# Kernel tuning notes

Measured on AMD Instinct MI355X. Metric: run time of the kernel, lower is better.

## Reference

```python
import jax, jax.numpy as jnp
import numpy as np

EPS = 1e-6

def _rms_norm(x, w):
    # per-head RMSNorm over last dim (head_dim)
    var = jnp.mean(jnp.square(x), axis=-1, keepdims=True)
    return x * jax.lax.rsqrt(var + EPS) * w

def _linear(x, w, b):
    # torch nn.Linear: y = x @ W^T + b
    return jnp.einsum('bsd,od->bso', x, w) + b

def setup_inputs() -> dict:
    key = jax.random.key(0)
    ks = jax.random.split(key, 16)
    B, S, S_enc, D, H, HD = 1, 2048, 256, 1536, 24, 64
    w = lambda k: jax.random.normal(k, (D, D), dtype=jnp.float32) * 0.02
    return {
        'hidden_states': jax.random.normal(ks[0], (B, S, D), dtype=jnp.float32),
        'encoder_hidden_states': jax.random.normal(ks[1], (B, S_enc, D), dtype=jnp.float32),
        'attention_mask': jnp.zeros((B, 1, 1, S + S_enc), dtype=jnp.float32),
        'to_q_weight': w(ks[2]), 'to_q_bias': jnp.zeros((D,), jnp.float32),
        'to_k_weight': w(ks[3]), 'to_k_bias': jnp.zeros((D,), jnp.float32),
        'to_v_weight': w(ks[4]), 'to_v_bias': jnp.zeros((D,), jnp.float32),
        'norm_q_weight': jnp.ones((HD,), jnp.float32),
        'norm_k_weight': jnp.ones((HD,), jnp.float32),
        'add_q_proj_weight': w(ks[5]), 'add_q_proj_bias': jnp.zeros((D,), jnp.float32),
        'add_k_proj_weight': w(ks[6]), 'add_k_proj_bias': jnp.zeros((D,), jnp.float32),
        'add_v_proj_weight': w(ks[7]), 'add_v_proj_bias': jnp.zeros((D,), jnp.float32),
        'norm_added_q_weight': jnp.ones((HD,), jnp.float32),
        'norm_added_k_weight': jnp.ones((HD,), jnp.float32),
        'to_out_0_weight': w(ks[8]), 'to_out_0_bias': jnp.zeros((D,), jnp.float32),
        'to_add_out_weight': w(ks[9]), 'to_add_out_bias': jnp.zeros((D,), jnp.float32),
        'attn_heads': 24,
        'attn_head_dim': 64,
    }

def reference(hidden_states, encoder_hidden_states, attention_mask,
              to_q_weight, to_q_bias, to_k_weight, to_k_bias, to_v_weight, to_v_bias,
              norm_q_weight, norm_k_weight,
              add_q_proj_weight, add_q_proj_bias, add_k_proj_weight, add_k_proj_bias,
              add_v_proj_weight, add_v_proj_bias,
              norm_added_q_weight, norm_added_k_weight,
              to_out_0_weight, to_out_0_bias, to_add_out_weight, to_add_out_bias,
              attn_heads, attn_head_dim):
    B, S, D = hidden_states.shape
    S_enc = encoder_hidden_states.shape[1]
    H, HD = attn_heads, attn_head_dim
    scale = float(HD) ** -0.5

    def split_heads(x):  # [B,T,H*HD] -> [B,H,T,HD]
        return x.reshape(B, -1, H, HD).transpose(0, 2, 1, 3)

    # hidden-stream QKV + per-head RMSNorm on q,k
    q = _rms_norm(split_heads(_linear(hidden_states, to_q_weight, to_q_bias)), norm_q_weight)
    k = _rms_norm(split_heads(_linear(hidden_states, to_k_weight, to_k_bias)), norm_k_weight)
    v = split_heads(_linear(hidden_states, to_v_weight, to_v_bias))

    # encoder-stream QKV + per-head RMSNorm on q,k
    eq = _rms_norm(split_heads(_linear(encoder_hidden_states, add_q_proj_weight, add_q_proj_bias)), norm_added_q_weight)
    ek = _rms_norm(split_heads(_linear(encoder_hidden_states, add_k_proj_weight, add_k_proj_bias)), norm_added_k_weight)
    ev = split_heads(_linear(encoder_hidden_states, add_v_proj_weight, add_v_proj_bias))

    # concat streams along sequence: [B,H,S+S_enc,HD]
    q = jnp.concatenate([q, eq], axis=2)
    k = jnp.concatenate([k, ek], axis=2)
    v = jnp.concatenate([v, ev], axis=2)

    # SDPA with additive mask
    scores = jnp.einsum('bhqd,bhkd->bhqk', q, k) * scale + attention_mask
    probs = jax.nn.softmax(scores, axis=-1)
    out = jnp.einsum('bhqk,bhkd->bhqd', probs, v)  # [B,H,T,HD]
    out = out.transpose(0, 2, 1, 3).reshape(B, S + S_enc, H * HD)

    # split back into image / text streams, separate output projections
    attn_output = _linear(out[:, :S], to_out_0_weight, to_out_0_bias)
    context_attn_output = _linear(out[:, S:], to_add_out_weight, to_add_out_bias)
    del context_attn_output  # AttentionFunc returns only the hidden-stream output
    return attn_output
```

## Files before the change

### kernel.cpp

```cpp
#include <hip/hip_runtime.h>
#include <cstdint>


typedef __attribute__((ext_vector_type(8))) short s16x8;
typedef __attribute__((ext_vector_type(4))) float f32x4;

#define LOG2E 1.4426950408889634f

__device__ __forceinline__ short f2bf(float f) {
  union { float f; uint32_t u; } v; v.f = f;
  uint32_t r = v.u + 0x7FFFu + ((v.u >> 16) & 1u);
  return (short)(r >> 16);
}
__device__ __forceinline__ short f2bf_fast(float f) {
  union { float f; uint32_t u; } v; v.f = f;
  return (short)((v.u + 0x8000u) >> 16);
}

typedef uint32_t __attribute__((address_space(1)))* gas_u32;
typedef uint32_t __attribute__((address_space(3)))* las_u32;

__device__ __forceinline__ void gload_lds16(const short* g, short* l) {
  __builtin_amdgcn_global_load_lds((gas_u32)(g), (las_u32)(l), 16, 0, 0);
}

struct CvtSeg { const float* src; short* dst; int n4; };
struct CvtArgs { CvtSeg s[8]; };

__global__ __launch_bounds__(256) void cvt_bf16_kernel(CvtArgs a) {
  const int stride = gridDim.x * blockDim.x;
  const int tid = blockIdx.x * blockDim.x + threadIdx.x;
  for (int i = 0; i < 8; ++i) {
    const float4* src = (const float4*)a.s[i].src;
    short* dst = a.s[i].dst;
    const int n4 = a.s[i].n4;
    for (int j = tid; j < n4; j += stride) {
      float4 v = src[j];
      short4 o;
      o.x = f2bf(v.x); o.y = f2bf(v.y); o.z = f2bf(v.z); o.w = f2bf(v.w);
      *(short4*)(dst + (size_t)j * 4) = o;
    }
  }
}

enum { MODE_Q = 0, MODE_K = 1, MODE_V = 2, MODE_OUT = 3 };

struct GemmCfg {
  const short* A;
  const short* W;
  const float* bias;
  const float* normw;
  void* dst;
  int toff;
  int mode;
  int mtiles;
};
struct GemmArgs { GemmCfg c[5]; };

__global__ __launch_bounds__(256) void proj_gemm_kernel(GemmArgs args) {
  const GemmCfg cfg = args.c[blockIdx.z];
  if ((int)blockIdx.y >= cfg.mtiles) return;
  constexpr int K = 1536;
  __shared__ short As[4096];
  __shared__ short Bs[4096];
  const int t = threadIdx.x;
  const int lane = t & 63;
  const int wave = t >> 6;
  const int l16 = lane & 15;
  const int quad = lane >> 4;
  const int wm = wave >> 1;
  const int wn = wave & 1;

  const short* __restrict__ Ag = cfg.A + (size_t)(blockIdx.y * 128) * K;
  const short* __restrict__ Wg = cfg.W + (size_t)(blockIdx.x * 128) * K;
  const int srow = t >> 2;
  const int scol = (t & 3) << 3;

  const f32x4 z4 = {0.f, 0.f, 0.f, 0.f};
  f32x4 acc[4][4];
#pragma unroll
  for (int i = 0; i < 4; ++i) {
#pragma unroll
    for (int j = 0; j < 4; ++j) acc[i][j] = z4;
  }

  for (int k0 = 0; k0 < K; k0 += 32) {
    gload_lds16(Ag + (size_t)srow * K + k0 + scol, As + t * 8);
    gload_lds16(Ag + (size_t)(srow + 64) * K + k0 + scol, As + 2048 + t * 8);
    gload_lds16(Wg + (size_t)srow * K + k0 + scol, Bs + t * 8);
    gload_lds16(Wg + (size_t)(srow + 64) * K + k0 + scol, Bs + 2048 + t * 8);
    __syncthreads();
    s16x8 af[4], bfr[4];
#pragma unroll
    for (int i = 0; i < 4; ++i)
      af[i] = *(const s16x8*)(As + (wm * 64 + i * 16 + l16) * 32 + quad * 8);
#pragma unroll
    for (int i = 0; i < 4; ++i)
      bfr[i] = *(const s16x8*)(Bs + (wn * 64 + i * 16 + l16) * 32 + quad * 8);
#pragma unroll
    for (int mi = 0; mi < 4; ++mi) {
#pragma unroll
      for (int ni = 0; ni < 4; ++ni)
        acc[mi][ni] = __builtin_amdgcn_mfma_f32_16x16x32_bf16(af[mi], bfr[ni], acc[mi][ni], 0, 0, 0);
    }
    __syncthreads();
  }

  const int nbase = blockIdx.x * 128 + wn * 64;
  const int mbase = blockIdx.y * 128 + wm * 64;
  const int mode = cfg.mode;
  const int h = nbase >> 6;

  float biasv[4], nwv[4];
#pragma unroll
  for (int ni = 0; ni < 4; ++ni) {
    int col = nbase + ni * 16 + l16;
    biasv[ni] = cfg.bias[col];
    nwv[ni] = (mode == MODE_Q || mode == MODE_K) ? cfg.normw[col & 63] : 0.f;
  }

#pragma unroll
  for (int mi = 0; mi < 4; ++mi) {
    float vv[4][4];
#pragma unroll
    for (int ni = 0; ni < 4; ++ni) {
#pragma unroll
      for (int r = 0; r < 4; ++r) vv[ni][r] = acc[mi][ni][r] + biasv[ni];
    }
    if (mode == MODE_Q || mode == MODE_K) {
      float ss[4];
#pragma unroll
      for (int r = 0; r < 4; ++r)
        ss[r] = vv[0][r] * vv[0][r] + vv[1][r] * vv[1][r] +
                vv[2][r] * vv[2][r] + vv[3][r] * vv[3][r];
#pragma unroll
      for (int r = 0; r < 4; ++r) {
        ss[r] += __shfl_xor(ss[r], 1);
        ss[r] += __shfl_xor(ss[r], 2);
        ss[r] += __shfl_xor(ss[r], 4);
        ss[r] += __shfl_xor(ss[r], 8);
        float rs = rsqrtf(ss[r] * (1.0f / 64.0f) + 1e-6f);
#pragma unroll
        for (int ni = 0; ni < 4; ++ni) vv[ni][r] *= rs * nwv[ni];
      }
    }
    const int row0 = mbase + mi * 16 + quad * 4;
    if (mode == MODE_Q) {
      short* Qd = (short*)cfg.dst;
#pragma unroll
      for (int ni = 0; ni < 4; ++ni) {
        int d = ni * 16 + l16;
#pragma unroll
        for (int r = 0; r < 4; ++r)
          Qd[((size_t)h * 2048 + row0 + r) * 64 + d] = f2bf(vv[ni][r]);
      }
    } else if (mode == MODE_K) {
      short* Kd = (short*)cfg.dst;
#pragma unroll
      for (int ni = 0; ni < 4; ++ni) {
        int d = ni * 16 + l16;
#pragma unroll
        for (int r = 0; r < 4; ++r)
          Kd[((size_t)h * 2304 + cfg.toff + row0 + r) * 64 + d] = f2bf(vv[ni][r]);
      }
    } else if (mode == MODE_V) {
      short* Vd = (short*)cfg.dst;
#pragma unroll
      for (int ni = 0; ni < 4; ++ni) {
        int d = ni * 16 + l16;
        short4 o4;
        o4.x = f2bf(vv[ni][0]); o4.y = f2bf(vv[ni][1]);
        o4.z = f2bf(vv[ni][2]); o4.w = f2bf(vv[ni][3]);
        *(short4*)(Vd + ((size_t)h * 64 + d) * 2304 + cfg.toff + row0) = o4;
      }
    } else {
      float* Od = (float*)cfg.dst;
#pragma unroll
      for (int ni = 0; ni < 4; ++ni) {
        int col = nbase + ni * 16 + l16;
#pragma unroll
        for (int r = 0; r < 4; ++r)
          Od[(size_t)(row0 + r) * 1536 + col] = vv[ni][r];
      }
    }
  }
}

__global__ __launch_bounds__(256) void flash_kernel(
    const short* __restrict__ Q, const short* __restrict__ Kc,
    const short* __restrict__ VT, const float* __restrict__ mask,
    short* __restrict__ AO) {
  const int b = blockIdx.x;
  const int h = (b & 7) * 3 + ((b >> 3) % 3);
  const int q0 = ((b >> 3) / 3) * 64;
  const int lane = threadIdx.x & 63;
  const int wave = threadIdx.x >> 6;
  const int qw = wave & 1;
  const int ks = wave >> 1;
  const int l16 = lane & 15;
  const int quad = lane >> 4;

  __shared__ __align__(16) short smem[20480];

  const short* Kh = Kc + (size_t)h * 2304 * 64;
  const short* Vh = VT + (size_t)h * 64 * 2304;

  s16x8 aq0[2], aq1[2];
#pragma unroll
  for (int g = 0; g < 2; ++g) {
    const short* Qrow =
        Q + ((size_t)h * 2048 + q0 + qw * 32 + g * 16 + l16) * 64;
    aq0[g] = *(const s16x8*)(Qrow + quad * 8);
    aq1[g] = *(const s16x8*)(Qrow + quad * 8 + 32);
  }

  s16x8 ones;
#pragma unroll
  for (int i = 0; i < 8; ++i) ones[i] = (short)0x3F80;

  const f32x4 z4 = {0.f, 0.f, 0.f, 0.f};
  f32x4 o[2][4];
#pragma unroll
  for (int g = 0; g < 2; ++g)
#pragma unroll
    for (int ni = 0; ni < 4; ++ni) o[g][ni] = z4;
  f32x4 lacc[2] = {z4, z4};
  const float SC = 0.125f * LOG2E;
  const int kbase = ks * 1152;

  auto stage = [&](int it, int buf) {
    const int kb = kbase + it * 32;
    short* kt = smem + (ks * 2 + buf) * 2048;
    short* vt = smem + 8192 + (ks * 2 + buf) * 2048;
#pragma unroll
    for (int c = 0; c < 2; ++c) {
      const int gi = c * 128 + qw * 64 + lane;
      const int trow = gi >> 3, cp = gi & 7;
      gload_lds16(Kh + (size_t)(kb + trow) * 64 + ((cp ^ (trow & 7)) << 3),
                  kt + c * 1024 + qw * 512 + lane * 8);
      const int d = gi >> 2, cpv = gi & 3;
      gload_lds16(Vh + (size_t)d * 2304 + kb + ((cpv ^ ((d >> 1) & 3)) << 3),
                  vt + c * 1024 + qw * 512 + lane * 8);
    }
  };

  stage(0, 0);
  __syncthreads();

  for (int it = 0; it < 36; ++it) {
    const int buf = it & 1;
    if (it < 35) stage(it + 1, buf ^ 1);
    const short* kt = smem + (ks * 2 + buf) * 2048;
    const short* vt = smem + 8192 + (ks * 2 + buf) * 2048;
    const int kb = kbase + it * 32;

    s16x8 bk[2][2];
#pragma unroll
    for (int ni = 0; ni < 2; ++ni) {
      const int tt = ni * 16 + l16;
      const short* kr = kt + tt * 64;
      bk[ni][0] = *(const s16x8*)(kr + ((quad ^ (tt & 7)) << 3));
      bk[ni][1] = *(const s16x8*)(kr + (((quad + 4) ^ (tt & 7)) << 3));
    }
    s16x8 bv[4];
#pragma unroll
    for (int ni = 0; ni < 4; ++ni) {
      const int d = ni * 16 + l16;
      bv[ni] = *(const s16x8*)(vt + d * 32 + ((quad ^ ((d >> 1) & 3)) << 3));
    }
    float mvl[2];
#pragma unroll
    for (int ni = 0; ni < 2; ++ni) mvl[ni] = mask[kb + ni * 16 + l16] * LOG2E;

#pragma unroll
    for (int g = 0; g < 2; ++g) {
      short* Pg = smem + 16384 + wave * 1024 + g * 512;
#pragma unroll
      for (int ni = 0; ni < 2; ++ni) {
        f32x4 s = __builtin_amdgcn_mfma_f32_16x16x32_bf16(aq0[g], bk[ni][0], z4, 0, 0, 0);
        s = __builtin_amdgcn_mfma_f32_16x16x32_bf16(aq1[g], bk[ni][1], s, 0, 0, 0);
        const int tt = ni * 16 + l16;
        const int cc = tt >> 3;
#pragma unroll
        for (int rr = 0; rr < 4; ++rr) {
          float pv = __builtin_amdgcn_exp2f(fmaf(s[rr], SC, mvl[ni]));
          const int prow = quad * 4 + rr;
          Pg[prow * 32 + ((cc ^ ((prow >> 1) & 3)) << 3) + (tt & 7)] = f2bf_fast(pv);
        }
      }
      s16x8 ap = *(const s16x8*)(Pg + l16 * 32 + ((quad ^ ((l16 >> 1) & 3)) << 3));
      lacc[g] = __builtin_amdgcn_mfma_f32_16x16x32_bf16(ap, ones, lacc[g], 0, 0, 0);
#pragma unroll
      for (int ni = 0; ni < 4; ++ni)
        o[g][ni] = __builtin_amdgcn_mfma_f32_16x16x32_bf16(ap, bv[ni], o[g][ni], 0, 0, 0);
    }
    __syncthreads();
  }

  f32x4* R = (f32x4*)smem;
  if (ks == 1) {
    f32x4* Rw = R + (qw * 64 + lane) * 10;
#pragma unroll
    for (int g = 0; g < 2; ++g) {
#pragma unroll
      for (int ni = 0; ni < 4; ++ni) Rw[g * 5 + ni] = o[g][ni];
      Rw[g * 5 + 4] = lacc[g];
    }
  }
  __syncthreads();
  if (ks == 0) {
    const f32x4* Rw = R + (qw * 64 + lane) * 10;
#pragma unroll
    for (int g = 0; g < 2; ++g) {
#pragma unroll
      for (int ni = 0; ni < 4; ++ni) o[g][ni] += Rw[g * 5 + ni];
      f32x4 ls = lacc[g] + Rw[g * 5 + 4];
#pragma unroll
      for (int rr = 0; rr < 4; ++rr) {
        float inv = 1.0f / ls[rr];
        int tq = q0 + qw * 32 + g * 16 + quad * 4 + rr;
#pragma unroll
        for (int ni = 0; ni < 4; ++ni)
          AO[(size_t)tq * 1536 + h * 64 + ni * 16 + l16] = f2bf(o[g][ni][rr] * inv);
      }
    }
  }
}

extern "C" void kernel_launch(void* const* d_in, const int* in_sizes, int n_in,
                              void* d_out, int out_size, void* d_ws, size_t ws_size,
                              hipStream_t stream) {
  (void)in_sizes; (void)n_in; (void)out_size; (void)ws_size;
  const float* hidden = (const float*)d_in[0];
  const float* enc    = (const float*)d_in[1];
  const float* amask  = (const float*)d_in[2];
  const float* wq  = (const float*)d_in[3];  const float* bq  = (const float*)d_in[4];
  const float* wk  = (const float*)d_in[5];  const float* bk  = (const float*)d_in[6];
  const float* wv  = (const float*)d_in[7];  const float* bv  = (const float*)d_in[8];
  const float* nqw = (const float*)d_in[9];  const float* nkw = (const float*)d_in[10];
  const float* wak = (const float*)d_in[13]; const float* bak = (const float*)d_in[14];
  const float* wav = (const float*)d_in[15]; const float* bav = (const float*)d_in[16];
  const float* nakw = (const float*)d_in[18];
  const float* wo  = (const float*)d_in[19]; const float* bo  = (const float*)d_in[20];
  float* out = (float*)d_out;

  char* p = (char*)d_ws;
  auto carve = [&](size_t bytes) { char* r = p; p += (bytes + 255) & ~(size_t)255; return r; };
  short* Xb   = (short*)carve((size_t)2048 * 1536 * 2);
  short* Eb   = (short*)carve((size_t)256 * 1536 * 2);
  short* Wqb  = (short*)carve((size_t)1536 * 1536 * 2);
  short* Wkb  = (short*)carve((size_t)1536 * 1536 * 2);
  short* Wvb  = (short*)carve((size_t)1536 * 1536 * 2);
  short* Wakb = (short*)carve((size_t)1536 * 1536 * 2);
  short* Wavb = (short*)carve((size_t)1536 * 1536 * 2);
  short* Wob  = (short*)carve((size_t)1536 * 1536 * 2);
  short* Qb   = (short*)carve((size_t)24 * 2048 * 64 * 2);
  short* Kb   = (short*)carve((size_t)24 * 2304 * 64 * 2);
  short* VTb  = (short*)carve((size_t)24 * 64 * 2304 * 2);
  short* AOb  = (short*)carve((size_t)2048 * 1536 * 2);

  CvtArgs ca;
  ca.s[0] = {hidden, Xb, 2048 * 1536 / 4};
  ca.s[1] = {enc,    Eb, 256 * 1536 / 4};
  ca.s[2] = {wq,  Wqb,  1536 * 1536 / 4};
  ca.s[3] = {wk,  Wkb,  1536 * 1536 / 4};
  ca.s[4] = {wv,  Wvb,  1536 * 1536 / 4};
  ca.s[5] = {wak, Wakb, 1536 * 1536 / 4};
  ca.s[6] = {wav, Wavb, 1536 * 1536 / 4};
  ca.s[7] = {wo,  Wob,  1536 * 1536 / 4};
  cvt_bf16_kernel<<<dim3(1024), dim3(256), 0, stream>>>(ca);

  GemmArgs g1;
  g1.c[0] = {Xb, Wqb,  bq,  nqw,     (void*)Qb,  0,    MODE_Q, 16};
  g1.c[1] = {Xb, Wkb,  bk,  nkw,     (void*)Kb,  0,    MODE_K, 16};
  g1.c[2] = {Xb, Wvb,  bv,  nullptr, (void*)VTb, 0,    MODE_V, 16};
  g1.c[3] = {Eb, Wakb, bak, nakw,    (void*)Kb,  2048, MODE_K, 2};
  g1.c[4] = {Eb, Wavb, bav, nullptr, (void*)VTb, 2048, MODE_V, 2};
  proj_gemm_kernel<<<dim3(12, 16, 5), dim3(256), 0, stream>>>(g1);

  flash_kernel<<<dim3(768), dim3(256), 0, stream>>>(Qb, Kb, VTb, amask, AOb);

  GemmArgs g3;
  g3.c[0] = {AOb, Wob, bo, nullptr, (void*)out, 0, MODE_OUT, 16};
  proj_gemm_kernel<<<dim3(12, 16, 1), dim3(256), 0, stream>>>(g3);
}
```

Baseline: 294.2 us.

## Compute transposed QK^T so P stays in registers, drop LDS round-trip

The QK^T MFMA now swaps operands so each lane holds scores along the key dimension, and the K rows staged into LDS are permuted to match. The exponentiated probabilities are packed to bf16 with v_cvt_pk_bf16_f32 and fed straight into the PV MFMA, removing the per-wave LDS write and read of P. The row sums become scalar per-lane accumulations reduced with shuffles at the end, replacing the extra MFMA against a ones vector. Shared memory shrinks and the mask is loaded as float4 vectors, but correctness now depends on the key-row permutation matching the MFMA register layout.

After: 290.3 us. No clear change (-1.3%).

```diff
diff --git a/kernel.cpp b/kernel.cpp
--- a/kernel.cpp
+++ b/kernel.cpp
@@ -12,9 +12,11 @@
   uint32_t r = v.u + 0x7FFFu + ((v.u >> 16) & 1u);
   return (short)(r >> 16);
 }
-__device__ __forceinline__ short f2bf_fast(float f) {
-  union { float f; uint32_t u; } v; v.f = f;
-  return (short)((v.u + 0x8000u) >> 16);
+
+__device__ __forceinline__ uint32_t cvt_pk_bf16(float lo, float hi) {
+  uint32_t r;
+  asm("v_cvt_pk_bf16_f32 %0, %1, %2" : "=v"(r) : "v"(lo), "v"(hi));
+  return r;
 }
 
 typedef uint32_t __attribute__((address_space(1)))* gas_u32;
@@ -200,7 +202,7 @@
   const int l16 = lane & 15;
   const int quad = lane >> 4;
 
-  __shared__ __align__(16) short smem[20480];
+  __shared__ __align__(16) short smem[16384];
 
   const short* Kh = Kc + (size_t)h * 2304 * 64;
   const short* Vh = VT + (size_t)h * 64 * 2304;
@@ -214,17 +216,13 @@
     aq1[g] = *(const s16x8*)(Qrow + quad * 8 + 32);
   }
 
-  s16x8 ones;
-#pragma unroll
-  for (int i = 0; i < 8; ++i) ones[i] = (short)0x3F80;
-
   const f32x4 z4 = {0.f, 0.f, 0.f, 0.f};
   f32x4 o[2][4];
 #pragma unroll
   for (int g = 0; g < 2; ++g)
 #pragma unroll
-    for (int ni = 0; ni < 4; ++ni) o[g][ni] = z4;
-  f32x4 lacc[2] = {z4, z4};
+    for (int mi = 0; mi < 4; ++mi) o[g][mi] = z4;
+  float lsum[2] = {0.f, 0.f};
   const float SC = 0.125f * LOG2E;
   const int kbase = ks * 1152;
 
@@ -236,7 +234,8 @@
     for (int c = 0; c < 2; ++c) {
       const int gi = c * 128 + qw * 64 + lane;
       const int trow = gi >> 3, cp = gi & 7;
-      gload_lds16(Kh + (size_t)(kb + trow) * 64 + ((cp ^ (trow & 7)) << 3),
+      const int srow = ((trow & 12) << 1) | ((trow & 16) >> 2) | (trow & 3);
+      gload_lds16(Kh + (size_t)(kb + srow) * 64 + ((cp ^ (trow & 7)) << 3),
                   kt + c * 1024 + qw * 512 + lane * 8);
       const int d = gi >> 2, cpv = gi & 3;
       gload_lds16(Vh + (size_t)d * 2304 + kb + ((cpv ^ ((d >> 1) & 3)) << 3),
@@ -264,64 +263,66 @@
     }
     s16x8 bv[4];
 #pragma unroll
-    for (int ni = 0; ni < 4; ++ni) {
-      const int d = ni * 16 + l16;
-      bv[ni] = *(const s16x8*)(vt + d * 32 + ((quad ^ ((d >> 1) & 3)) << 3));
-    }
-    float mvl[2];
-#pragma unroll
-    for (int ni = 0; ni < 2; ++ni) mvl[ni] = mask[kb + ni * 16 + l16] * LOG2E;
+    for (int mi = 0; mi < 4; ++mi) {
+      const int d = mi * 16 + l16;
+      bv[mi] = *(const s16x8*)(vt + d * 32 + ((quad ^ ((d >> 1) & 3)) << 3));
+    }
+    float4 mv0 = *(const float4*)(mask + kb + quad * 8);
+    float4 mv1 = *(const float4*)(mask + kb + quad * 8 + 4);
+    const float m8[8] = {mv0.x * LOG2E, mv0.y * LOG2E, mv0.z * LOG2E, mv0.w * LOG2E,
+                         mv1.x * LOG2E, mv1.y * LOG2E, mv1.z * LOG2E, mv1.w * LOG2E};
 
 #pragma unroll
     for (int g = 0; g < 2; ++g) {
-      short* Pg = smem + 16384 + wave * 1024 + g * 512;
+      union { uint32_t w[4]; s16x8 v; } pu;
 #pragma unroll
       for (int ni = 0; ni < 2; ++ni) {
-        f32x4 s = __builtin_amdgcn_mfma_f32_16x16x32_bf16(aq0[g], bk[ni][0], z4, 0, 0, 0);
-        s = __builtin_amdgcn_mfma_f32_16x16x32_bf16(aq1[g], bk[ni][1], s, 0, 0, 0);
-        const int tt = ni * 16 + l16;
-        const int cc = tt >> 3;
-#pragma unroll
-        for (int rr = 0; rr < 4; ++rr) {
-          float pv = __builtin_amdgcn_exp2f(fmaf(s[rr], SC, mvl[ni]));
-          const int prow = quad * 4 + rr;
-          Pg[prow * 32 + ((cc ^ ((prow >> 1) & 3)) << 3) + (tt & 7)] = f2bf_fast(pv);
-        }
-      }
-      s16x8 ap = *(const s16x8*)(Pg + l16 * 32 + ((quad ^ ((l16 >> 1) & 3)) << 3));
-      lacc[g] = __builtin_amdgcn_mfma_f32_16x16x32_bf16(ap, ones, lacc[g], 0, 0, 0);
-#pragma unroll
-      for (int ni = 0; ni < 4; ++ni)
-        o[g][ni] = __builtin_amdgcn_mfma_f32_16x16x32_bf16(ap, bv[ni], o[g][ni], 0, 0, 0);
+        f32x4 s = __builtin_amdgcn_mfma_f32_16x16x32_bf16(bk[ni][0], aq0[g], z4, 0, 0, 0);
+        s = __builtin_amdgcn_mfma_f32_16x16x32_bf16(bk[ni][1], aq1[g], s, 0, 0, 0);
+        float p[4];
+#pragma unroll
+        for (int rr = 0; rr < 4; ++rr)
+          p[rr] = __builtin_amdgcn_exp2f(fmaf(s[rr], SC, m8[ni * 4 + rr]));
+        lsum[g] += (p[0] + p[1]) + (p[2] + p[3]);
+        pu.w[ni * 2 + 0] = cvt_pk_bf16(p[0], p[1]);
+        pu.w[ni * 2 + 1] = cvt_pk_bf16(p[2], p[3]);
+      }
+#pragma unroll
+      for (int mi = 0; mi < 4; ++mi)
+        o[g][mi] = __builtin_amdgcn_mfma_f32_16x16x32_bf16(pu.v, bv[mi], o[g][mi], 0, 0, 0);
     }
     __syncthreads();
   }
 
   f32x4* R = (f32x4*)smem;
+  float* L = (float*)(smem + 8192);
   if (ks == 1) {
-    f32x4* Rw = R + (qw * 64 + lane) * 10;
-#pragma unroll
-    for (int g = 0; g < 2; ++g) {
-#pragma unroll
-      for (int ni = 0; ni < 4; ++ni) Rw[g * 5 + ni] = o[g][ni];
-      Rw[g * 5 + 4] = lacc[g];
-    }
+    f32x4* Rw = R + (qw * 64 + lane) * 8;
+#pragma unroll
+    for (int g = 0; g < 2; ++g)
+#pragma unroll
+      for (int mi = 0; mi < 4; ++mi) Rw[g * 4 + mi] = o[g][mi];
+    L[(qw * 64 + lane) * 2 + 0] = lsum[0];
+    L[(qw * 64 + lane) * 2 + 1] = lsum[1];
   }
   __syncthreads();
   if (ks == 0) {
-    const f32x4* Rw = R + (qw * 64 + lane) * 10;
+    const f32x4* Rw = R + (qw * 64 + lane) * 8;
 #pragma unroll
     for (int g = 0; g < 2; ++g) {
 #pragma unroll
-      for (int ni = 0; ni < 4; ++ni) o[g][ni] += Rw[g * 5 + ni];
-      f32x4 ls = lacc[g] + Rw[g * 5 + 4];
+      for (int mi = 0; mi < 4; ++mi) o[g][mi] += Rw[g * 4 + mi];
+      float lf = lsum[g] + L[(qw * 64 + lane) * 2 + g];
+      lf += __shfl_xor(lf, 16);
+      lf += __shfl_xor(lf, 32);
 #pragma unroll
       for (int rr = 0; rr < 4; ++rr) {
-        float inv = 1.0f / ls[rr];
+        float lq = __shfl(lf, (lane & 48) | (quad * 4 + rr));
+        float inv = 1.0f / lq;
         int tq = q0 + qw * 32 + g * 16 + quad * 4 + rr;
 #pragma unroll
-        for (int ni = 0; ni < 4; ++ni)
-          AO[(size_t)tq * 1536 + h * 64 + ni * 16 + l16] = f2bf(o[g][ni][rr] * inv);
+        for (int mi = 0; mi < 4; ++mi)
+          AO[(size_t)tq * 1536 + h * 64 + mi * 16 + l16] = f2bf(o[g][mi][rr] * inv);
       }
     }
   }
```
